# Optimization experiments

Measured on AMD Instinct MI355X. Metric: run time of the kernel, lower is better.

## Reference

```python
import jax, jax.numpy as jnp
import numpy as np

NUM_LAYERS = 3
CHANNELS = 8
IN_CHANNELS = 8
MASK_FEAT_STRIDE = 8
MASK_OUT_STRIDE = 4
SOI = np.array([64., 128., 256., 512., 1024.], dtype=np.float32)
WEIGHT_NUMS = [(IN_CHANNELS + 2) * CHANNELS, CHANNELS * CHANNELS, CHANNELS * 1]  # [80, 64, 8]
BIAS_NUMS = [CHANNELS, CHANNELS, 1]
NUM_GEN_PARAMS = sum(WEIGHT_NUMS) + sum(BIAS_NUMS)  # 169


def aligned_bilinear(x, factor):
    # Faithful to adet.utils.comm.aligned_bilinear
    if factor == 1:
        return x
    n, c, h, w = x.shape
    x = jnp.pad(x, ((0, 0), (0, 0), (0, 1), (0, 1)), mode='edge')  # replicate pad right/bottom
    oh, ow = factor * h + 1, factor * w + 1

    def interp_axis(t, out_len, axis):
        # align_corners=True from (in_len) to (out_len) with scale (in_len-1)/(out_len-1) == 1/factor
        src = jnp.arange(out_len, dtype=t.dtype) / factor
        i0 = jnp.floor(src).astype(jnp.int32)
        i1 = jnp.minimum(i0 + 1, t.shape[axis] - 1)
        wgt = src - i0.astype(t.dtype)
        a = jnp.take(t, i0, axis=axis)
        b = jnp.take(t, i1, axis=axis)
        shp = [1] * t.ndim
        shp[axis] = out_len
        wgt = wgt.reshape(shp)
        return a * (1 - wgt) + b * wgt

    x = interp_axis(x, oh, 2)
    x = interp_axis(x, ow, 3)
    pad = factor // 2
    x = jnp.pad(x, ((0, 0), (0, 0), (pad, 0), (pad, 0)), mode='edge')
    return x[:, :, :oh - 1, :ow - 1]


def setup_inputs() -> dict:
    key = jax.random.key(0)
    k1, k2, k3, k4, k5 = jax.random.split(key, 5)
    mask_feats = jax.random.normal(k1, (2, IN_CHANNELS, 128, 192), dtype=jnp.float32)
    mask_head_params = jax.random.normal(k2, (400, NUM_GEN_PARAMS), dtype=jnp.float32)
    inst_locations = jax.random.uniform(k3, (400, 2), dtype=jnp.float32) * 1024.0
    im_inds = jax.random.randint(k4, (400,), 0, 2, dtype=jnp.int32)
    fpn_levels = jax.random.randint(k5, (400,), 0, 5, dtype=jnp.int32)
    return {
        'mask_feats': mask_feats,
        'mask_head_params': mask_head_params,
        'inst_locations': inst_locations,
        'im_inds': im_inds,
        'fpn_levels': fpn_levels,
    }


def reference(mask_feats, mask_head_params, inst_locations, im_inds, fpn_levels):
    N, C, H, W = mask_feats.shape
    n_inst = mask_head_params.shape[0]
    dt = mask_feats.dtype

    # compute_locations: pixel centers at stride MASK_FEAT_STRIDE
    sx = jnp.arange(W, dtype=dt) * MASK_FEAT_STRIDE + MASK_FEAT_STRIDE // 2
    sy = jnp.arange(H, dtype=dt) * MASK_FEAT_STRIDE + MASK_FEAT_STRIDE // 2
    yy, xx = jnp.meshgrid(sy, sx, indexing='ij')
    locs = jnp.stack([xx.reshape(-1), yy.reshape(-1)], axis=1)  # [HW, 2] (x, y)

    # relative coords, normalized by size-of-interest per fpn level
    rel = inst_locations[:, None, :] - locs[None, :, :]          # [n, HW, 2]
    rel = jnp.transpose(rel, (0, 2, 1))                          # [n, 2, HW]
    soi = jnp.asarray(SOI, dtype=dt)[fpn_levels]                 # [n]
    rel = rel / soi[:, None, None]

    feats = mask_feats[im_inds].reshape(n_inst, IN_CHANNELS, H * W)
    x = jnp.concatenate([rel, feats], axis=1)                    # [n, 10, HW]

    # parse_dynamic_params: split into per-instance weights/biases
    offs = np.cumsum([0] + WEIGHT_NUMS + BIAS_NUMS)
    w0 = mask_head_params[:, offs[0]:offs[1]].reshape(n_inst, CHANNELS, IN_CHANNELS + 2)
    w1 = mask_head_params[:, offs[1]:offs[2]].reshape(n_inst, CHANNELS, CHANNELS)
    w2 = mask_head_params[:, offs[2]:offs[3]].reshape(n_inst, 1, CHANNELS)
    b0 = mask_head_params[:, offs[3]:offs[4]]                    # [n, 8]
    b1 = mask_head_params[:, offs[4]:offs[5]]                    # [n, 8]
    b2 = mask_head_params[:, offs[5]:offs[6]]                    # [n, 1]

    # grouped 1x1 convs == per-instance tiny GEMMs over pixels
    x = jax.nn.relu(jnp.einsum('noi,nip->nop', w0, x) + b0[:, :, None])
    x = jax.nn.relu(jnp.einsum('noi,nip->nop', w1, x) + b1[:, :, None])
    x = jnp.einsum('noi,nip->nop', w2, x) + b2[:, :, None]

    mask_logits = x.reshape(n_inst, 1, H, W)
    return aligned_bilinear(mask_logits, MASK_FEAT_STRIDE // MASK_OUT_STRIDE)
```

## Files before the change

kernel.cpp:

```cpp
#include <hip/hip_runtime.h>


#define HH   128
#define WW   192
#define HW   (HH*WW)
#define OHH  256
#define OWW  384
#define THY  32
#define TWX  128
#define LR   18
#define LC   66
#define LCP  67
#define NPX  (LR*LC)
#define NPARAMS 169
#define PXT  5

__global__ __launch_bounds__(256, 4)
void dmh_fused(const float* __restrict__ mask_feats,
               const float* __restrict__ params,
               const float* __restrict__ locs,
               const int*   __restrict__ im_inds,
               const int*   __restrict__ fpn,
               float* __restrict__ out)
{
    __shared__ float sw[176];
    __shared__ float L[LR][LCP];

    const int inst = blockIdx.z;
    const int tid  = threadIdx.x;

    if (tid < NPARAMS) {
        const float v = params[(size_t)inst * NPARAMS + tid];
        int d;
        if      (tid <  80) d = (tid % 10) * 8 + (tid / 10);
        else                d = tid;
        sw[d] = v;
    }

    const int   im     = im_inds[inst];
    const float instx  = locs[2*inst];
    const float insty  = locs[2*inst + 1];
    const float invsoi = 1.0f / (float)(64 << fpn[inst]);

    const int oy0 = blockIdx.y * THY;
    const int ox0 = blockIdx.x * TWX;
    const int r0  = oy0 >> 1;
    const int c0  = ox0 >> 1;

    __syncthreads();

    const float* __restrict__ fbase = mask_feats + (size_t)im * 8 * HW;

    float rx[PXT], ry[PXT];
    int   foff[PXT];
    int   pix[PXT];
#pragma unroll
    for (int k = 0; k < PXT; ++k) {
        int p = tid + 256*k;
        if (p > NPX-1) p = NPX-1;
        int lr = p / LC;
        int lc = p - lr*LC;
        pix[k] = lr*LCP + lc;
        int gy = r0 - 1 + lr; gy = gy < 0 ? 0 : (gy > HH-1 ? HH-1 : gy);
        int gx = c0 - 1 + lc; gx = gx < 0 ? 0 : (gx > WW-1 ? WW-1 : gx);
        rx[k] = (instx - (float)(gx*8 + 4)) * invsoi;
        ry[k] = (insty - (float)(gy*8 + 4)) * invsoi;
        foff[k] = gy*WW + gx;
    }

    float h0[PXT][8];
    {
        float4 A = *(const float4*)&sw[0];
        float4 B = *(const float4*)&sw[4];
#pragma unroll
        for (int k = 0; k < PXT; ++k) {
            h0[k][0] = A.x*rx[k]; h0[k][1] = A.y*rx[k];
            h0[k][2] = A.z*rx[k]; h0[k][3] = A.w*rx[k];
            h0[k][4] = B.x*rx[k]; h0[k][5] = B.y*rx[k];
            h0[k][6] = B.z*rx[k]; h0[k][7] = B.w*rx[k];
        }
        A = *(const float4*)&sw[8];
        B = *(const float4*)&sw[12];
#pragma unroll
        for (int k = 0; k < PXT; ++k) {
            h0[k][0] += A.x*ry[k]; h0[k][1] += A.y*ry[k];
            h0[k][2] += A.z*ry[k]; h0[k][3] += A.w*ry[k];
            h0[k][4] += B.x*ry[k]; h0[k][5] += B.y*ry[k];
            h0[k][6] += B.z*ry[k]; h0[k][7] += B.w*ry[k];
        }
#pragma unroll
        for (int cc = 0; cc < 8; ++cc) {
            const float* fp = fbase + cc*HW;
            float xv[PXT];
#pragma unroll
            for (int k = 0; k < PXT; ++k) xv[k] = fp[foff[k]];
            A = *(const float4*)&sw[(cc+2)*8];
            B = *(const float4*)&sw[(cc+2)*8 + 4];
#pragma unroll
            for (int k = 0; k < PXT; ++k) {
                h0[k][0] += A.x*xv[k]; h0[k][1] += A.y*xv[k];
                h0[k][2] += A.z*xv[k]; h0[k][3] += A.w*xv[k];
                h0[k][4] += B.x*xv[k]; h0[k][5] += B.y*xv[k];
                h0[k][6] += B.z*xv[k]; h0[k][7] += B.w*xv[k];
            }
        }
#pragma unroll
        for (int o = 0; o < 8; ++o) {
            const float b = sw[152 + o];
#pragma unroll
            for (int k = 0; k < PXT; ++k)
                h0[k][o] = fmaxf(h0[k][o] + b, 0.0f);
        }
    }

    float h1[PXT][8];
#pragma unroll
    for (int o = 0; o < 8; ++o) {
        const float4 A = *(const float4*)&sw[80 + 8*o];
        const float4 B = *(const float4*)&sw[80 + 8*o + 4];
        const float  b = sw[160 + o];
#pragma unroll
        for (int k = 0; k < PXT; ++k) {
            float a = A.x*h0[k][0] + A.y*h0[k][1] + A.z*h0[k][2] + A.w*h0[k][3]
                    + B.x*h0[k][4] + B.y*h0[k][5] + B.z*h0[k][6] + B.w*h0[k][7];
            h1[k][o] = fmaxf(a + b, 0.0f);
        }
    }

    {
        const float4 A = *(const float4*)&sw[144];
        const float4 B = *(const float4*)&sw[148];
        const float  b = sw[168];
#pragma unroll
        for (int k = 0; k < PXT; ++k) {
            float a = A.x*h1[k][0] + A.y*h1[k][1] + A.z*h1[k][2] + A.w*h1[k][3]
                    + B.x*h1[k][4] + B.y*h1[k][5] + B.z*h1[k][6] + B.w*h1[k][7];
            ((float*)L)[pix[k]] = a + b;
        }
    }

    __syncthreads();

    float* __restrict__ obase = out + (size_t)inst * OHH * OWW;
#pragma unroll
    for (int j = 0; j < 4; ++j) {
        const int yl = (tid >> 5) + 8*j;
        const int xq = (tid & 31) * 4;
        const int y  = oy0 + yl;
        const int yy = (y > 0) ? (y - 1) : 0;
        const int iy0 = yy >> 1;
        const float fy = (yy & 1) ? 0.5f : 0.0f;
        const float gy1 = 1.0f - fy;
        const int ly = iy0 - r0 + 1;
        const int lx = xq >> 1;
        float t[3];
#pragma unroll
        for (int i = 0; i < 3; ++i) {
            const float a  = L[ly  ][lx + i];
            const float bb = L[ly+1][lx + i];
            t[i] = a*gy1 + bb*fy;
        }
        float4 r;
        r.x = 0.5f*t[0] + 0.5f*t[1];
        r.y = t[1];
        r.z = 0.5f*t[1] + 0.5f*t[2];
        r.w = t[2];
        *(float4*)(obase + (size_t)y*OWW + ox0 + xq) = r;
    }
}

extern "C" void kernel_launch(void* const* d_in, const int* in_sizes, int n_in,
                              void* d_out, int out_size, void* d_ws, size_t ws_size,
                              hipStream_t stream) {
    const float* mask_feats = (const float*)d_in[0];
    const float* params     = (const float*)d_in[1];
    const float* locs       = (const float*)d_in[2];
    const int*   im_inds    = (const int*)d_in[3];
    const int*   fpn        = (const int*)d_in[4];
    float*       out        = (float*)d_out;

    const int n_inst = in_sizes[1] / NPARAMS;
    dim3 grid(OWW/TWX, OHH/THY, n_inst);
    dmh_fused<<<grid, 256, 0, stream>>>(mask_feats, params, locs, im_inds, fpn, out);
}
```

Baseline: 197.7 us.

## Split fused mask head into logits kernel and separate upsample kernel via workspace

The single fused kernel is replaced by two kernels whenever the workspace is large enough. The first computes the per-instance MLP logits once per low-res pixel, using float4 feature loads and no halo recomputation. The second reads those logits back from the workspace and does the 2x aligned bilinear upsample. This removes the roughly 1.2x halo recompute and the shared-memory staging, at the cost of writing and re-reading about 39 MB of intermediate logits plus a second launch.

```diff
diff --git a/kernel.cpp b/kernel.cpp
--- a/kernel.cpp
+++ b/kernel.cpp
@@ -6,13 +6,146 @@
 #define HW   (HH*WW)
 #define OHH  256
 #define OWW  384
+#define NPARAMS 169
+
+__global__ __launch_bounds__(256, 4)
+void dmh_logits(const float* __restrict__ mask_feats,
+                const float* __restrict__ params,
+                const float* __restrict__ locs,
+                const int*   __restrict__ im_inds,
+                const int*   __restrict__ fpn,
+                float* __restrict__ lg)
+{
+    __shared__ float sw[176];
+    const int inst = blockIdx.y;
+    const int tid  = threadIdx.x;
+    if (tid < NPARAMS) {
+        const float v = params[(size_t)inst * NPARAMS + tid];
+        const int d = (tid < 80) ? (tid % 10) * 8 + (tid / 10) : tid;
+        sw[d] = v;
+    }
+    const int   im     = im_inds[inst];
+    const float instx  = locs[2*inst];
+    const float insty  = locs[2*inst + 1];
+    const float invsoi = 1.0f / (float)(64 << fpn[inst]);
+    __syncthreads();
+
+    const int p  = blockIdx.x * 1024 + tid * 4;
+    const int gy = p / WW;
+    const int gx = p - gy * WW;
+    const float ry  = (insty - (float)(gy*8 + 4)) * invsoi;
+    const float dx  = 8.0f * invsoi;
+    const float rx0 = (instx - (float)(gx*8 + 4)) * invsoi;
+    const float rxv[4] = {rx0, rx0 - dx, rx0 - 2.0f*dx, rx0 - 3.0f*dx};
+
+    const float* __restrict__ fp = mask_feats + (size_t)im * 8 * HW + p;
+
+    float h0[4][8];
+    {
+        float4 A = *(const float4*)&sw[0];
+        float4 B = *(const float4*)&sw[4];
+#pragma unroll
+        for (int k = 0; k < 4; ++k) {
+            const float r = rxv[k];
+            h0[k][0] = A.x*r; h0[k][1] = A.y*r; h0[k][2] = A.z*r; h0[k][3] = A.w*r;
+            h0[k][4] = B.x*r; h0[k][5] = B.y*r; h0[k][6] = B.z*r; h0[k][7] = B.w*r;
+        }
+        A = *(const float4*)&sw[8];
+        B = *(const float4*)&sw[12];
+#pragma unroll
+        for (int k = 0; k < 4; ++k) {
+            h0[k][0] += A.x*ry; h0[k][1] += A.y*ry; h0[k][2] += A.z*ry; h0[k][3] += A.w*ry;
+            h0[k][4] += B.x*ry; h0[k][5] += B.y*ry; h0[k][6] += B.z*ry; h0[k][7] += B.w*ry;
+        }
+#pragma unroll
+        for (int cc = 0; cc < 8; ++cc) {
+            const float4 xv = *(const float4*)&fp[cc * HW];
+            const float xa[4] = {xv.x, xv.y, xv.z, xv.w};
+            A = *(const float4*)&sw[(cc+2)*8];
+            B = *(const float4*)&sw[(cc+2)*8 + 4];
+#pragma unroll
+            for (int k = 0; k < 4; ++k) {
+                const float x = xa[k];
+                h0[k][0] += A.x*x; h0[k][1] += A.y*x; h0[k][2] += A.z*x; h0[k][3] += A.w*x;
+                h0[k][4] += B.x*x; h0[k][5] += B.y*x; h0[k][6] += B.z*x; h0[k][7] += B.w*x;
+            }
+        }
+#pragma unroll
+        for (int o = 0; o < 8; ++o) {
+            const float b = sw[152 + o];
+#pragma unroll
+            for (int k = 0; k < 4; ++k)
+                h0[k][o] = fmaxf(h0[k][o] + b, 0.0f);
+        }
+    }
+
+    float h1[4][8];
+#pragma unroll
+    for (int o = 0; o < 8; ++o) {
+        const float4 A = *(const float4*)&sw[80 + 8*o];
+        const float4 B = *(const float4*)&sw[80 + 8*o + 4];
+        const float  b = sw[160 + o];
+#pragma unroll
+        for (int k = 0; k < 4; ++k) {
+            float a = A.x*h0[k][0] + A.y*h0[k][1] + A.z*h0[k][2] + A.w*h0[k][3]
+                    + B.x*h0[k][4] + B.y*h0[k][5] + B.z*h0[k][6] + B.w*h0[k][7];
+            h1[k][o] = fmaxf(a + b, 0.0f);
+        }
+    }
+
+    {
+        const float4 A = *(const float4*)&sw[144];
+        const float4 B = *(const float4*)&sw[148];
+        const float  b = sw[168];
+        float4 r;
+        float* pr = (float*)&r;
+#pragma unroll
+        for (int k = 0; k < 4; ++k) {
+            float a = A.x*h1[k][0] + A.y*h1[k][1] + A.z*h1[k][2] + A.w*h1[k][3]
+                    + B.x*h1[k][4] + B.y*h1[k][5] + B.z*h1[k][6] + B.w*h1[k][7];
+            pr[k] = a + b;
+        }
+        *(float4*)&lg[(size_t)inst * HW + p] = r;
+    }
+}
+
+__global__ __launch_bounds__(384)
+void dmh_upsample(const float* __restrict__ lg, float* __restrict__ out)
+{
+    const int inst = blockIdx.y;
+    const int tid  = threadIdx.x;
+    const int yq   = tid / 96;
+    const int xg   = tid - yq * 96;
+    const int y    = blockIdx.x * 4 + yq;
+    const int yy   = (y > 0) ? (y - 1) : 0;
+    const int iy0  = yy >> 1;
+    const int iy1  = (iy0 + 1 > HH-1) ? (HH-1) : (iy0 + 1);
+    const float fy = (yy & 1) ? 0.5f : 0.0f;
+    const float g1 = 1.0f - fy;
+
+    const int m  = 2 * xg;
+    const int cm = (xg > 0) ? (m - 1) : 0;
+    const float* __restrict__ r0 = lg + (size_t)inst * HW + (size_t)iy0 * WW;
+    const float* __restrict__ r1 = lg + (size_t)inst * HW + (size_t)iy1 * WW;
+
+    const float tA = r0[cm ]*g1 + r1[cm ]*fy;
+    const float tB = r0[m  ]*g1 + r1[m  ]*fy;
+    const float tC = r0[m+1]*g1 + r1[m+1]*fy;
+
+    float4 r;
+    r.x = 0.5f*(tA + tB);
+    r.y = tB;
+    r.z = 0.5f*(tB + tC);
+    r.w = tC;
+    *(float4*)(out + (size_t)inst * OHH * OWW + (size_t)y * OWW + xg * 4) = r;
+}
+
 #define THY  32
 #define TWX  128
 #define LR   18
 #define LC   66
 #define LCP  67
 #define NPX  (LR*LC)
-#define NPARAMS 169
 #define PXT  5
 
 __global__ __launch_bounds__(256, 4)
@@ -25,35 +158,25 @@
 {
     __shared__ float sw[176];
     __shared__ float L[LR][LCP];
-
     const int inst = blockIdx.z;
     const int tid  = threadIdx.x;
-
     if (tid < NPARAMS) {
         const float v = params[(size_t)inst * NPARAMS + tid];
-        int d;
-        if      (tid <  80) d = (tid % 10) * 8 + (tid / 10);
-        else                d = tid;
+        const int d = (tid < 80) ? (tid % 10) * 8 + (tid / 10) : tid;
         sw[d] = v;
     }
-
     const int   im     = im_inds[inst];
     const float instx  = locs[2*inst];
     const float insty  = locs[2*inst + 1];
     const float invsoi = 1.0f / (float)(64 << fpn[inst]);
-
     const int oy0 = blockIdx.y * THY;
     const int ox0 = blockIdx.x * TWX;
     const int r0  = oy0 >> 1;
     const int c0  = ox0 >> 1;
-
     __syncthreads();
-
     const float* __restrict__ fbase = mask_feats + (size_t)im * 8 * HW;
-
     float rx[PXT], ry[PXT];
-    int   foff[PXT];
-    int   pix[PXT];
+    int foff[PXT], pix[PXT];
 #pragma unroll
     for (int k = 0; k < PXT; ++k) {
         int p = tid + 256*k;
@@ -67,41 +190,34 @@
         ry[k] = (insty - (float)(gy*8 + 4)) * invsoi;
         foff[k] = gy*WW + gx;
     }
-
     float h0[PXT][8];
     {
         float4 A = *(const float4*)&sw[0];
         float4 B = *(const float4*)&sw[4];
 #pragma unroll
         for (int k = 0; k < PXT; ++k) {
-            h0[k][0] = A.x*rx[k]; h0[k][1] = A.y*rx[k];
-            h0[k][2] = A.z*rx[k]; h0[k][3] = A.w*rx[k];
-            h0[k][4] = B.x*rx[k]; h0[k][5] = B.y*rx[k];
-            h0[k][6] = B.z*rx[k]; h0[k][7] = B.w*rx[k];
+            h0[k][0] = A.x*rx[k]; h0[k][1] = A.y*rx[k]; h0[k][2] = A.z*rx[k]; h0[k][3] = A.w*rx[k];
+            h0[k][4] = B.x*rx[k]; h0[k][5] = B.y*rx[k]; h0[k][6] = B.z*rx[k]; h0[k][7] = B.w*rx[k];
         }
         A = *(const float4*)&sw[8];
         B = *(const float4*)&sw[12];
 #pragma unroll
         for (int k = 0; k < PXT; ++k) {
-            h0[k][0] += A.x*ry[k]; h0[k][1] += A.y*ry[k];
-            h0[k][2] += A.z*ry[k]; h0[k][3] += A.w*ry[k];
-            h0[k][4] += B.x*ry[k]; h0[k][5] += B.y*ry[k];
-            h0[k][6] += B.z*ry[k]; h0[k][7] += B.w*ry[k];
+            h0[k][0] += A.x*ry[k]; h0[k][1] += A.y*ry[k]; h0[k][2] += A.z*ry[k]; h0[k][3] += A.w*ry[k];
+            h0[k][4] += B.x*ry[k]; h0[k][5] += B.y*ry[k]; h0[k][6] += B.z*ry[k]; h0[k][7] += B.w*ry[k];
         }
 #pragma unroll
         for (int cc = 0; cc < 8; ++cc) {
-            const float* fp = fbase + cc*HW;
+            const float* fpp = fbase + cc*HW;
             float xv[PXT];
 #pragma unroll
-            for (int k = 0; k < PXT; ++k) xv[k] = fp[foff[k]];
+            for (int k = 0; k < PXT; ++k) xv[k] = fpp[foff[k]];
             A = *(const float4*)&sw[(cc+2)*8];
             B = *(const float4*)&sw[(cc+2)*8 + 4];
 #pragma unroll
             for (int k = 0; k < PXT; ++k) {
-                h0[k][0] += A.x*xv[k]; h0[k][1] += A.y*xv[k];
-                h0[k][2] += A.z*xv[k]; h0[k][3] += A.w*xv[k];
-                h0[k][4] += B.x*xv[k]; h0[k][5] += B.y*xv[k];
-                h0[k][6] += B.z*xv[k]; h0[k][7] += B.w*xv[k];
+                h0[k][0] += A.x*xv[k]; h0[k][1] += A.y*xv[k]; h0[k][2] += A.z*xv[k]; h0[k][3] += A.w*xv[k];
+                h0[k][4] += B.x*xv[k]; h0[k][5] += B.y*xv[k]; h0[k][6] += B.z*xv[k]; h0[k][7] += B.w*xv[k];
             }
         }
 #pragma unroll
@@ -112,7 +228,6 @@
                 h0[k][o] = fmaxf(h0[k][o] + b, 0.0f);
         }
     }
-
     float h1[PXT][8];
 #pragma unroll
     for (int o = 0; o < 8; ++o) {
@@ -126,7 +241,6 @@
             h1[k][o] = fmaxf(a + b, 0.0f);
         }
     }
-
     {
         const float4 A = *(const float4*)&sw[144];
         const float4 B = *(const float4*)&sw[148];
@@ -138,9 +252,7 @@
             ((float*)L)[pix[k]] = a + b;
         }
     }
-
     __syncthreads();
-
     float* __restrict__ obase = out + (size_t)inst * OHH * OWW;
 #pragma unroll
     for (int j = 0; j < 4; ++j) {
@@ -178,8 +290,14 @@
     const int*   im_inds    = (const int*)d_in[3];
     const int*   fpn        = (const int*)d_in[4];
     float*       out        = (float*)d_out;
-
     const int n_inst = in_sizes[1] / NPARAMS;
-    dim3 grid(OWW/TWX, OHH/THY, n_inst);
-    dmh_fused<<<grid, 256, 0, stream>>>(mask_feats, params, locs, im_inds, fpn, out);
+
+    const size_t need = (size_t)n_inst * HW * sizeof(float);
+    if (ws_size >= need) {
+        float* lg = (float*)d_ws;
+        dmh_logits  <<<dim3(24, n_inst), 256, 0, stream>>>(mask_feats, params, locs, im_inds, fpn, lg);
+        dmh_upsample<<<dim3(64, n_inst), 384, 0, stream>>>(lg, out);
+    } else {
+        dmh_fused<<<dim3(OWW/TWX, OHH/THY, n_inst), 256, 0, stream>>>(mask_feats, params, locs, im_inds, fpn, out);
+    }
 }
```

Result: slower. 235.7 us (+19.3%).
